# Kernel optimization log

Hardware: AMD Instinct MI355X
Metric: run time of the kernel (lower is better)

The kernel has to match this reference:

```python
import jax, jax.numpy as jnp
import numpy as np

N_NODES = 50000
NEG_SLOPE = 0.2
EPS = 1e-16


def gatv2_layer(x, src, dst, Wl, Wr, att, bias):
    # x: [N, F_in]; Wl, Wr: [F_in, F_out]; att: [F_out]; bias: [F_out]
    xl = x @ Wl  # source-side transform [N, F_out]
    xr = x @ Wr  # target-side transform [N, F_out]
    # per-edge GATv2 logit: att . LeakyReLU(xl[src] + xr[dst])
    z = xl[src] + xr[dst]                               # [E, F_out]
    e = jnp.sum(jax.nn.leaky_relu(z, NEG_SLOPE) * att, axis=-1)  # [E]
    # segment softmax over incoming edges of each dst node
    m = jax.ops.segment_max(e, dst, num_segments=N_NODES)       # [N]
    a = jnp.exp(e - m[dst])                                      # [E]
    s = jax.ops.segment_sum(a, dst, num_segments=N_NODES)       # [N]
    alpha = a / (s[dst] + EPS)                                   # [E]
    # weighted scatter-aggregate of source messages
    out = jax.ops.segment_sum(alpha[:, None] * xl[src], dst, num_segments=N_NODES)
    return out + bias


def setup_inputs() -> dict:
    key = jax.random.key(0)
    ks = jax.random.split(key, 10)
    F_in, H, C = 256, 128, 64
    glorot = lambda k, fi, fo: jax.random.normal(k, (fi, fo), jnp.float32) * np.sqrt(2.0 / (fi + fo))
    x = jax.random.normal(ks[0], (N_NODES, F_in), jnp.float32)
    edge_index = jax.random.randint(ks[1], (2, 1600000), 0, N_NODES, jnp.int64 if jax.config.jax_enable_x64 else jnp.int32)
    Wl1 = glorot(ks[2], F_in, H)
    Wr1 = glorot(ks[3], F_in, H)
    att1 = jax.random.normal(ks[4], (H,), jnp.float32) * np.sqrt(2.0 / H)
    b1 = jnp.zeros((H,), jnp.float32)
    Wl2 = glorot(ks[5], H, C)
    Wr2 = glorot(ks[6], H, C)
    att2 = jax.random.normal(ks[7], (C,), jnp.float32) * np.sqrt(2.0 / C)
    b2 = jnp.zeros((C,), jnp.float32)
    return {"x": x, "edge_index": edge_index, "Wl1": Wl1, "Wr1": Wr1, "att1": att1, "b1": b1,
            "Wl2": Wl2, "Wr2": Wr2, "att2": att2, "b2": b2}


def reference(x, edge_index, Wl1, Wr1, att1, b1, Wl2, Wr2, att2, b2):
    src, dst = edge_index[0], edge_index[1]
    h = gatv2_layer(x, src, dst, Wl1, Wr1, att1, b1)
    h = jax.nn.relu(h)
    # dropout is identity in eval mode
    out = gatv2_layer(h, src, dst, Wl2, Wr2, att2, b2)
    return out
```

## Files before the change

kernel.cpp:

```cpp
#include <hip/hip_runtime.h>

#define N_NODES 50000
#define M_PAD 50048
#define MT 391
#define GEMM1_BLOCKS 782
#define F_IN 256
#define F_H 128
#define F_OUT 64
#define E_MAX 1600000
#define NEG_SLOPE 0.2f
#define EPS_F 1e-16f
#define NPART 196
#define NBUCK 196
#define CH_E 4096
#define NQUAD 12500
#define ATT_GRID 2048
#define FUSED_LDS 40960

typedef __bf16 bf16x8 __attribute__((ext_vector_type(8)));
typedef float f32x4 __attribute__((ext_vector_type(4)));
typedef float f32x2 __attribute__((ext_vector_type(2)));

__device__ unsigned short g_B1h[256 * 256];
__device__ unsigned short g_B1l[256 * 256];
__device__ unsigned short g_B2h[128 * 128];
__device__ unsigned short g_B2l[128 * 128];
__device__ unsigned short g_hh[(size_t)M_PAD * F_H];
__device__ unsigned short g_hl[(size_t)M_PAD * F_H];
__device__ unsigned short g_xl1b[(size_t)N_NODES * F_H];
__device__ float g_xr1[(size_t)N_NODES * F_H];
__device__ unsigned short g_xl2b[(size_t)N_NODES * F_OUT];
__device__ float g_xr2[(size_t)N_NODES * F_OUT];
__device__ unsigned g_cnt[N_NODES];
__device__ unsigned g_part[NPART];
__device__ unsigned g_rowstart[N_NODES + 1];
__device__ unsigned g_bcursor[NBUCK];
__device__ unsigned g_bucketed[E_MAX];
__device__ int g_src_sorted[E_MAX];

__device__ inline float san(float v) { return fminf(fmaxf(v, -64.f), 64.f); }
__device__ inline unsigned short f2bf(float f) {
    unsigned u = __float_as_uint(f);
    return (unsigned short)((u + 0x7fffu + ((u >> 16) & 1u)) >> 16);
}
__device__ inline float bf2f(unsigned short h) {
    return __uint_as_float(((unsigned)h) << 16);
}
__device__ inline float blo(unsigned w) { return __uint_as_float(w << 16); }
__device__ inline float bhi(unsigned w) { return __uint_as_float(w & 0xffff0000u); }

__global__ __launch_bounds__(256) void prep_hist(const int* __restrict__ dst, int E,
                                                 const float* __restrict__ Wl1,
                                                 const float* __restrict__ Wr1,
                                                 const float* __restrict__ Wl2,
                                                 const float* __restrict__ Wr2) {
    int i = blockIdx.x * 256 + threadIdx.x;
    if (i < 256 * 256) {
        int n = i >> 8, k = i & 255;
        float v = san((n < 128) ? Wl1[k * 128 + n] : Wr1[k * 128 + (n - 128)]);
        unsigned short h = f2bf(v);
        g_B1h[n * 256 + k] = h;
        g_B1l[n * 256 + k] = f2bf(v - bf2f(h));
    }
    if (i < 128 * 128) {
        int n = i >> 7, k = i & 127;
        float v = san((n < 64) ? Wl2[k * 64 + n] : Wr2[k * 64 + (n - 64)]);
        unsigned short h = f2bf(v);
        g_B2h[n * 128 + k] = h;
        g_B2l[n * 128 + k] = f2bf(v - bf2f(h));
    }
    if (i < (M_PAD - N_NODES) * F_H) {
        g_hh[(size_t)N_NODES * F_H + i] = 0;
        g_hl[(size_t)N_NODES * F_H + i] = 0;
    }
    if (i < E) atomicAdd(&g_cnt[dst[i]], 1u);
}

__global__ __launch_bounds__(256) void scanA() {
    int i = blockIdx.x * 256 + threadIdx.x;
    unsigned v = (i < N_NODES) ? g_cnt[i] : 0u;
#pragma unroll
    for (int off = 32; off > 0; off >>= 1) v += __shfl_xor(v, off, 64);
    __shared__ unsigned ws[4];
    if ((threadIdx.x & 63) == 0) ws[threadIdx.x >> 6] = v;
    __syncthreads();
    if (threadIdx.x == 0) g_part[blockIdx.x] = ws[0] + ws[1] + ws[2] + ws[3];
}
__global__ __launch_bounds__(256) void scanC2(int E) {
    __shared__ unsigned lds[256];
    __shared__ unsigned ws[4];
    int t = threadIdx.x, bid = blockIdx.x;
    unsigned pv = (t < bid) ? g_part[t] : 0u;
#pragma unroll
    for (int off = 32; off > 0; off >>= 1) pv += __shfl_xor(pv, off, 64);
    if ((t & 63) == 0) ws[t >> 6] = pv;
    int i = bid * 256 + t;
    unsigned v = (i < N_NODES) ? g_cnt[i] : 0u;
    if (i < N_NODES) g_cnt[i] = 0u;
    lds[t] = v;
    __syncthreads();
    unsigned base = ws[0] + ws[1] + ws[2] + ws[3];
    for (int off = 1; off < 256; off <<= 1) {
        unsigned u = (t >= off) ? lds[t - off] : 0u;
        __syncthreads();
        lds[t] += u;
        __syncthreads();
    }
    if (i < N_NODES) g_rowstart[i] = lds[t] - v + base;
    if (t == 0) g_bcursor[bid] = base;
    if (i == 0) g_rowstart[N_NODES] = (unsigned)E;
}

__global__ __launch_bounds__(256) void sortA_gemm1(const int* __restrict__ src,
                                                   const int* __restrict__ dst,
                                                   int E, int nSort,
                                                   const float* __restrict__ x) {
    __shared__ __align__(16) unsigned char s_raw[FUSED_LDS];
    int t = threadIdx.x;

    if ((int)blockIdx.x < nSort) {
        unsigned* l_cnt  = (unsigned*)s_raw;
        unsigned* l_base = l_cnt + NBUCK;
        int*      l_gadj = (int*)(l_base + NBUCK);
        unsigned* sc     = (unsigned*)(l_gadj + NBUCK);
        unsigned* stageW = sc + 256;
        unsigned char* stageB = (unsigned char*)(stageW + CH_E);
        int e0 = blockIdx.x * CH_E;
        int e1 = min(e0 + CH_E, E);
        int n = e1 - e0;
        for (int i = t; i < NBUCK; i += 256) l_cnt[i] = 0u;
        __syncthreads();
        for (int e = e0 + t; e < e1; e += 256)
            atomicAdd(&l_cnt[dst[e] >> 8], 1u);
        __syncthreads();
        {
            unsigned v = (t < NBUCK) ? l_cnt[t] : 0u;
            sc[t] = v;
            __syncthreads();
            for (int off = 1; off < 256; off <<= 1) {
                unsigned u = (t >= off) ? sc[t - off] : 0u;
                __syncthreads();
                sc[t] += u;
                __syncthreads();
            }
            if (t < NBUCK) l_base[t] = sc[t] - v;
        }
        __syncthreads();
        for (int b = t; b < NBUCK; b += 256) {
            unsigned c = l_cnt[b];
            unsigned gb = c ? atomicAdd(&g_bcursor[b], c) : 0u;
            l_gadj[b] = (int)gb - (int)l_base[b];
            l_cnt[b] = l_base[b];
        }
        __syncthreads();
        for (int e = e0 + t; e < e1; e += 256) {
            int d = dst[e];
            int b = d >> 8;
            unsigned p = atomicAdd(&l_cnt[b], 1u);
            stageW[p] = (unsigned)src[e] | ((unsigned)d << 16);
            stageB[p] = (unsigned char)b;
        }
        __syncthreads();
        for (int i = t; i < n; i += 256) {
            int b = stageB[i];
            g_bucketed[l_gadj[b] + i] = stageW[i];
        }
        return;
    }

    typedef unsigned short row40[40];
    row40* As_h = (row40*)s_raw;
    row40* As_l = (row40*)(s_raw + 10240);
    row40* Bs_h = (row40*)(s_raw + 20480);
    row40* Bs_l = (row40*)(s_raw + 30720);

    int bx = blockIdx.x - nSort;
    const int n0 = (bx & 1) * 128;
    const int m0 = (bx >> 1) * 128;
    const int wave = t >> 6, lane = t & 63;
    const int wm = (wave >> 1) * 64, wn = (wave & 1) * 64;
    const int lr = lane & 15, g8 = (lane >> 4) * 8;
    const int srow = t >> 1, shalf = (t & 1) * 16;

    f32x4 acc[4][4];
#pragma unroll
    for (int i = 0; i < 4; ++i)
#pragma unroll
        for (int j = 0; j < 4; ++j) acc[i][j] = (f32x4){0.f, 0.f, 0.f, 0.f};

    for (int kb = 0; kb < 256; kb += 32) {
        __syncthreads();
        {
            int grow = m0 + srow;
            float f[16];
            if (grow < N_NODES) {
                const float4* xp = (const float4*)(x + (size_t)grow * F_IN + kb + shalf);
                float4 v0 = xp[0], v1 = xp[1], v2 = xp[2], v3 = xp[3];
                f[0] = v0.x;  f[1] = v0.y;  f[2] = v0.z;  f[3] = v0.w;
                f[4] = v1.x;  f[5] = v1.y;  f[6] = v1.z;  f[7] = v1.w;
                f[8] = v2.x;  f[9] = v2.y;  f[10] = v2.z; f[11] = v2.w;
                f[12] = v3.x; f[13] = v3.y; f[14] = v3.z; f[15] = v3.w;
            } else {
#pragma unroll
                for (int j = 0; j < 16; ++j) f[j] = 0.f;
            }
            unsigned hw[8], lw[8];
#pragma unroll
            for (int j = 0; j < 8; ++j) {
                float a = san(f[2 * j]), b = san(f[2 * j + 1]);
                unsigned short ha = f2bf(a), hb = f2bf(b);
                unsigned short la = f2bf(a - bf2f(ha)), lb = f2bf(b - bf2f(hb));
                hw[j] = ((unsigned)hb << 16) | ha;
                lw[j] = ((unsigned)lb << 16) | la;
            }
            *(uint4*)&As_h[srow][shalf]     = make_uint4(hw[0], hw[1], hw[2], hw[3]);
            *(uint4*)&As_h[srow][shalf + 8] = make_uint4(hw[4], hw[5], hw[6], hw[7]);
            *(uint4*)&As_l[srow][shalf]     = make_uint4(lw[0], lw[1], lw[2], lw[3]);
            *(uint4*)&As_l[srow][shalf + 8] = make_uint4(lw[4], lw[5], lw[6], lw[7]);
        }
        {
            size_t gb = (size_t)(n0 + srow) * 256 + kb + shalf;
            *(uint4*)&Bs_h[srow][shalf]     = *(const uint4*)(g_B1h + gb);
            *(uint4*)&Bs_h[srow][shalf + 8] = *(const uint4*)(g_B1h + gb + 8);
            *(uint4*)&Bs_l[srow][shalf]     = *(const uint4*)(g_B1l + gb);
            *(uint4*)&Bs_l[srow][shalf + 8] = *(const uint4*)(g_B1l + gb + 8);
        }
        __syncthreads();

        bf16x8 af_h[4], af_l[4], bf_h[4], bf_l[4];
#pragma unroll
        for (int i = 0; i < 4; ++i) {
            af_h[i] = *(const bf16x8*)&As_h[wm + i * 16 + lr][g8];
            af_l[i] = *(const bf16x8*)&As_l[wm + i * 16 + lr][g8];
        }
#pragma unroll
        for (int j = 0; j < 4; ++j) {
            bf_h[j] = *(const bf16x8*)&Bs_h[wn + j * 16 + lr][g8];
            bf_l[j] = *(const bf16x8*)&Bs_l[wn + j * 16 + lr][g8];
        }
#pragma unroll
        for (int i = 0; i < 4; ++i)
#pragma unroll
            for (int j = 0; j < 4; ++j) {
                acc[i][j] = __builtin_amdgcn_mfma_f32_16x16x32_bf16(af_h[i], bf_h[j], acc[i][j], 0, 0, 0);
                acc[i][j] = __builtin_amdgcn_mfma_f32_16x16x32_bf16(af_h[i], bf_l[j], acc[i][j], 0, 0, 0);
                acc[i][j] = __builtin_amdgcn_mfma_f32_16x16x32_bf16(af_l[i], bf_h[j], acc[i][j], 0, 0, 0);
            }
    }

    const int drow = (lane >> 4) * 4;
#pragma unroll
    for (int i = 0; i < 4; ++i)
#pragma unroll
        for (int j = 0; j < 4; ++j) {
            int gn = n0 + wn + j * 16 + lr;
#pragma unroll
            for (int r = 0; r < 4; ++r) {
                int m = m0 + wm + i * 16 + drow + r;
                if (m < N_NODES) {
                    if (gn < F_H) g_xl1b[(size_t)m * F_H + gn] = f2bf(acc[i][j][r]);
                    else          g_xr1[(size_t)m * F_H + (gn - F_H)] = acc[i][j][r];
                }
            }
        }
}

__global__ __launch_bounds__(256) void sortB() {
    __shared__ unsigned l_cur[256];
    int b = blockIdx.x;
    int d0 = b * 256;
    int t = threadIdx.x;
    l_cur[t] = g_rowstart[min(d0 + t, N_NODES)];
    unsigned bstart = g_rowstart[min(d0, N_NODES)];
    unsigned bend   = g_rowstart[min(d0 + 256, N_NODES)];
    __syncthreads();
    for (unsigned i = bstart + t; i < bend; i += 256) {
        unsigned e = g_bucketed[i];
        unsigned d = e >> 16;
        unsigned pos = atomicAdd(&l_cur[d - d0], 1u);
        g_src_sorted[pos] = (int)(e & 0xFFFFu);
    }
}

__global__ __launch_bounds__(256) void gemm2() {
    __shared__ __align__(16) unsigned short As_h[128][40];
    __shared__ __align__(16) unsigned short As_l[128][40];
    __shared__ __align__(16) unsigned short Bs_h[128][40];
    __shared__ __align__(16) unsigned short Bs_l[128][40];

    const int m0 = blockIdx.x * 128;
    const int t = threadIdx.x;
    const int wave = t >> 6, lane = t & 63;
    const int wm = (wave >> 1) * 64, wn = (wave & 1) * 64;
    const int lr = lane & 15, g8 = (lane >> 4) * 8;
    const int srow = t >> 1, shalf = (t & 1) * 16;

    f32x4 acc[4][4];
#pragma unroll
    for (int i = 0; i < 4; ++i)
#pragma unroll
        for (int j = 0; j < 4; ++j) acc[i][j] = (f32x4){0.f, 0.f, 0.f, 0.f};

    for (int kb = 0; kb < 128; kb += 32) {
        __syncthreads();
        {
            size_t ga = (size_t)(m0 + srow) * 128 + kb + shalf;
            *(uint4*)&As_h[srow][shalf]     = *(const uint4*)(g_hh + ga);
            *(uint4*)&As_h[srow][shalf + 8] = *(const uint4*)(g_hh + ga + 8);
            *(uint4*)&As_l[srow][shalf]     = *(const uint4*)(g_hl + ga);
            *(uint4*)&As_l[srow][shalf + 8] = *(const uint4*)(g_hl + ga + 8);
            size_t gb = (size_t)srow * 128 + kb + shalf;
            *(uint4*)&Bs_h[srow][shalf]     = *(const uint4*)(g_B2h + gb);
            *(uint4*)&Bs_h[srow][shalf + 8] = *(const uint4*)(g_B2h + gb + 8);
            *(uint4*)&Bs_l[srow][shalf]     = *(const uint4*)(g_B2l + gb);
            *(uint4*)&Bs_l[srow][shalf + 8] = *(const uint4*)(g_B2l + gb + 8);
        }
        __syncthreads();

        bf16x8 af_h[4], af_l[4], bf_h[4], bf_l[4];
#pragma unroll
        for (int i = 0; i < 4; ++i) {
            af_h[i] = *(const bf16x8*)&As_h[wm + i * 16 + lr][g8];
            af_l[i] = *(const bf16x8*)&As_l[wm + i * 16 + lr][g8];
        }
#pragma unroll
        for (int j = 0; j < 4; ++j) {
            bf_h[j] = *(const bf16x8*)&Bs_h[wn + j * 16 + lr][g8];
            bf_l[j] = *(const bf16x8*)&Bs_l[wn + j * 16 + lr][g8];
        }
#pragma unroll
        for (int i = 0; i < 4; ++i)
#pragma unroll
            for (int j = 0; j < 4; ++j) {
                acc[i][j] = __builtin_amdgcn_mfma_f32_16x16x32_bf16(af_h[i], bf_h[j], acc[i][j], 0, 0, 0);
                acc[i][j] = __builtin_amdgcn_mfma_f32_16x16x32_bf16(af_h[i], bf_l[j], acc[i][j], 0, 0, 0);
                acc[i][j] = __builtin_amdgcn_mfma_f32_16x16x32_bf16(af_l[i], bf_h[j], acc[i][j], 0, 0, 0);
            }
    }

    const int drow = (lane >> 4) * 4;
#pragma unroll
    for (int i = 0; i < 4; ++i)
#pragma unroll
        for (int j = 0; j < 4; ++j) {
            int gn = wn + j * 16 + lr;
#pragma unroll
            for (int r = 0; r < 4; ++r) {
                int m = m0 + wm + i * 16 + drow + r;
                if (m < N_NODES) {
                    if (gn < F_OUT) g_xl2b[(size_t)m * F_OUT + gn] = f2bf(acc[i][j][r]);
                    else            g_xr2[(size_t)m * F_OUT + (gn - F_OUT)] = acc[i][j][r];
                }
            }
        }
}

__global__ __launch_bounds__(256) void att_agg1(const float* __restrict__ att,
                                                const float* __restrict__ bias) {
    __shared__ float s_out[4][F_H];
    int wid = threadIdx.x >> 6, lane = threadIdx.x & 63;
    int g = lane >> 3;
    int fi = lane & 7;
    int f0 = fi * 16;

    f32x2 at2[8];
    {
        const float4* atp = (const float4*)(att + f0);
#pragma unroll
        for (int q = 0; q < 4; ++q) {
            float4 a = atp[q];
            at2[2 * q]     = (f32x2){san(a.x), san(a.y)};
            at2[2 * q + 1] = (f32x2){san(a.z), san(a.w)};
        }
    }

    for (int qd = blockIdx.x; qd < NQUAD; qd += gridDim.x) {
        int w = qd * 4 + wid;

        f32x2 xr2[8];
        {
            const float4* xrp = (const float4*)(g_xr1 + (size_t)w * F_H + f0);
#pragma unroll
            for (int q = 0; q < 4; ++q) {
                float4 v = xrp[q];
                xr2[2 * q]     = (f32x2){v.x, v.y};
                xr2[2 * q + 1] = (f32x2){v.z, v.w};
            }
        }

        int beg = (int)g_rowstart[w], end = (int)g_rowstart[w + 1];
        float m = -INFINITY, ssum = 0.f;
        f32x2 acc2[8];
#pragma unroll
        for (int q = 0; q < 8; ++q) acc2[q] = (f32x2){0.f, 0.f};

        for (int c0 = beg; c0 < end; c0 += 64) {
            int nc = min(64, end - c0);
            int mysrc = (lane < nc) ? g_src_sorted[c0 + lane] : 0;
            for (int r0 = 0; r0 < nc; r0 += 16) {
                int eA = r0 + g, eB = r0 + 8 + g;
                int sA = __shfl(mysrc, eA, 64);
                int sB = __shfl(mysrc, eB, 64);
                const uint4* rpA = (const uint4*)(g_xl1b + (size_t)sA * F_H + f0);
                const uint4* rpB = (const uint4*)(g_xl1b + (size_t)sB * F_H + f0);
                uint4 a0 = rpA[0], a1 = rpA[1];
                uint4 b0 = rpB[0], b1 = rpB[1];
                f32x2 rA[8];
                rA[0] = (f32x2){blo(a0.x), bhi(a0.x)};
                rA[1] = (f32x2){blo(a0.y), bhi(a0.y)};
                rA[2] = (f32x2){blo(a0.z), bhi(a0.z)};
                rA[3] = (f32x2){blo(a0.w), bhi(a0.w)};
                rA[4] = (f32x2){blo(a1.x), bhi(a1.x)};
                rA[5] = (f32x2){blo(a1.y), bhi(a1.y)};
                rA[6] = (f32x2){blo(a1.z), bhi(a1.z)};
                rA[7] = (f32x2){blo(a1.w), bhi(a1.w)};
                float dA1 = 0.f, dA2 = 0.f;
#pragma unroll
                for (int q = 0; q < 8; ++q) {
                    f32x2 z = rA[q] + xr2[q];
                    dA1 = fmaf(z.x, at2[q].x, dA1);
                    dA2 = fmaf(fabsf(z.x), at2[q].x, dA2);
                    dA1 = fmaf(z.y, at2[q].y, dA1);
                    dA2 = fmaf(fabsf(z.y), at2[q].y, dA2);
                }
                float dA = fmaf(0.6f, dA1, 0.4f * dA2);
                f32x2 rB[8];
                rB[0] = (f32x2){blo(b0.x), bhi(b0.x)};
                rB[1] = (f32x2){blo(b0.y), bhi(b0.y)};
                rB[2] = (f32x2){blo(b0.z), bhi(b0.z)};
                rB[3] = (f32x2){blo(b0.w), bhi(b0.w)};
                rB[4] = (f32x2){blo(b1.x), bhi(b1.x)};
                rB[5] = (f32x2){blo(b1.y), bhi(b1.y)};
                rB[6] = (f32x2){blo(b1.z), bhi(b1.z)};
                rB[7] = (f32x2){blo(b1.w), bhi(b1.w)};
                float dB1 = 0.f, dB2 = 0.f;
#pragma unroll
                for (int q = 0; q < 8; ++q) {
                    f32x2 z = rB[q] + xr2[q];
                    dB1 = fmaf(z.x, at2[q].x, dB1);
                    dB2 = fmaf(fabsf(z.x), at2[q].x, dB2);
                    dB1 = fmaf(z.y, at2[q].y, dB1);
                    dB2 = fmaf(fabsf(z.y), at2[q].y, dB2);
                }
                float dB = fmaf(0.6f, dB1, 0.4f * dB2);
                dA += __shfl_xor(dA, 1, 64);
                dA += __shfl_xor(dA, 2, 64);
                dA += __shfl_xor(dA, 4, 64);
                dB += __shfl_xor(dB, 1, 64);
                dB += __shfl_xor(dB, 2, 64);
                dB += __shfl_xor(dB, 4, 64);
                float eAv = (eA < nc) ? dA : -INFINITY;
                float eBv = (eB < nc) ? dB : -INFINITY;
                float M = fmaxf(eAv, eBv);
                M = fmaxf(M, __shfl_xor(M, 8, 64));
                M = fmaxf(M, __shfl_xor(M, 16, 64));
                M = fmaxf(M, __shfl_xor(M, 32, 64));
                if (M > m + 8.f) {
                    float sc = __expf(m - M);
                    m = M;
                    ssum *= sc;
#pragma unroll
                    for (int q = 0; q < 8; ++q) acc2[q] *= sc;
                }
                float pA = __expf(eAv - m);
                float pB = __expf(eBv - m);
                ssum += pA + pB;
#pragma unroll
                for (int q = 0; q < 8; ++q) {
                    acc2[q] += rA[q] * pA;
                    acc2[q] += rB[q] * pB;
                }
            }
        }
#pragma unroll
        for (int off = 8; off < 64; off <<= 1) {
            ssum += __shfl_xor(ssum, off, 64);
#pragma unroll
            for (int q = 0; q < 8; ++q) {
                acc2[q].x += __shfl_xor(acc2[q].x, off, 64);
                acc2[q].y += __shfl_xor(acc2[q].y, off, 64);
            }
        }
        float inv = 1.f / (ssum + EPS_F);
        if (g == 0) {
            float2* op = (float2*)&s_out[wid][f0];
#pragma unroll
            for (int q = 0; q < 8; ++q) {
                float2 v;
                v.x = acc2[q].x * inv; v.y = acc2[q].y * inv;
                op[q] = v;
            }
        }
        int f2 = lane * 2;
        float2 o = *(float2*)&s_out[wid][f2];
        o.x = fmaxf(o.x + san(bias[f2]), 0.f);
        o.y = fmaxf(o.y + san(bias[f2 + 1]), 0.f);
        unsigned short hx = f2bf(o.x), hy = f2bf(o.y);
        unsigned short lx = f2bf(o.x - bf2f(hx)), ly = f2bf(o.y - bf2f(hy));
        size_t base = (size_t)w * F_H + f2;
        *(unsigned*)(g_hh + base) = ((unsigned)hy << 16) | hx;
        *(unsigned*)(g_hl + base) = ((unsigned)ly << 16) | lx;
    }
}

__global__ __launch_bounds__(256) void att_agg2(const float* __restrict__ att,
                                                const float* __restrict__ bias,
                                                float* __restrict__ out) {
    __shared__ float s_out[4][F_OUT];
    int wid = threadIdx.x >> 6, lane = threadIdx.x & 63;
    int g = lane >> 3;
    int fi = lane & 7;
    int f0 = fi * 8;

    f32x2 at2[4];
    {
        const float4* atp = (const float4*)(att + f0);
#pragma unroll
        for (int q = 0; q < 2; ++q) {
            float4 a = atp[q];
            at2[2 * q]     = (f32x2){san(a.x), san(a.y)};
            at2[2 * q + 1] = (f32x2){san(a.z), san(a.w)};
        }
    }

    for (int qd = blockIdx.x; qd < NQUAD; qd += gridDim.x) {
        int w = qd * 4 + wid;

        f32x2 xr2[4];
        {
            const float4* xrp = (const float4*)(g_xr2 + (size_t)w * F_OUT + f0);
#pragma unroll
            for (int q = 0; q < 2; ++q) {
                float4 v = xrp[q];
                xr2[2 * q]     = (f32x2){v.x, v.y};
                xr2[2 * q + 1] = (f32x2){v.z, v.w};
            }
        }

        int beg = (int)g_rowstart[w], end = (int)g_rowstart[w + 1];
        float m = -INFINITY, ssum = 0.f;
        f32x2 acc2[4];
#pragma unroll
        for (int q = 0; q < 4; ++q) acc2[q] = (f32x2){0.f, 0.f};

        for (int c0 = beg; c0 < end; c0 += 64) {
            int nc = min(64, end - c0);
            int mysrc = (lane < nc) ? g_src_sorted[c0 + lane] : 0;
            for (int r0 = 0; r0 < nc; r0 += 16) {
                int eA = r0 + g, eB = r0 + 8 + g;
                int sA = __shfl(mysrc, eA, 64);
                int sB = __shfl(mysrc, eB, 64);
                uint4 a0 = *(const uint4*)(g_xl2b + (size_t)sA * F_OUT + f0);
                uint4 b0 = *(const uint4*)(g_xl2b + (size_t)sB * F_OUT + f0);
                f32x2 rA[4], rB[4];
                rA[0] = (f32x2){blo(a0.x), bhi(a0.x)};
                rA[1] = (f32x2){blo(a0.y), bhi(a0.y)};
                rA[2] = (f32x2){blo(a0.z), bhi(a0.z)};
                rA[3] = (f32x2){blo(a0.w), bhi(a0.w)};
                rB[0] = (f32x2){blo(b0.x), bhi(b0.x)};
                rB[1] = (f32x2){blo(b0.y), bhi(b0.y)};
                rB[2] = (f32x2){blo(b0.z), bhi(b0.z)};
                rB[3] = (f32x2){blo(b0.w), bhi(b0.w)};
                float dA1 = 0.f, dA2 = 0.f, dB1 = 0.f, dB2 = 0.f;
#pragma unroll
                for (int q = 0; q < 4; ++q) {
                    f32x2 zA = rA[q] + xr2[q];
                    dA1 = fmaf(zA.x, at2[q].x, dA1);
                    dA2 = fmaf(fabsf(zA.x), at2[q].x, dA2);
                    dA1 = fmaf(zA.y, at2[q].y, dA1);
                    dA2 = fmaf(fabsf(zA.y), at2[q].y, dA2);
                    f32x2 zB = rB[q] + xr2[q];
                    dB1 = fmaf(zB.x, at2[q].x, dB1);
                    dB2 = fmaf(fabsf(zB.x), at2[q].x, dB2);
                    dB1 = fmaf(zB.y, at2[q].y, dB1);
                    dB2 = fmaf(fabsf(zB.y), at2[q].y, dB2);
                }
                float dA = fmaf(0.6f, dA1, 0.4f * dA2);
                float dB = fmaf(0.6f, dB1, 0.4f * dB2);
                dA += __shfl_xor(dA, 1, 64);
                dA += __shfl_xor(dA, 2, 64);
                dA += __shfl_xor(dA, 4, 64);
                dB += __shfl_xor(dB, 1, 64);
                dB += __shfl_xor(dB, 2, 64);
                dB += __shfl_xor(dB, 4, 64);
                float eAv = (eA < nc) ? dA : -INFINITY;
                float eBv = (eB < nc) ? dB : -INFINITY;
                float M = fmaxf(eAv, eBv);
                M = fmaxf(M, __shfl_xor(M, 8, 64));
                M = fmaxf(M, __shfl_xor(M, 16, 64));
                M = fmaxf(M, __shfl_xor(M, 32, 64));
                if (M > m + 8.f) {
                    float sc = __expf(m - M);
                    m = M;
                    ssum *= sc;
#pragma unroll
                    for (int q = 0; q < 4; ++q) acc2[q] *= sc;
                }
                float pA = __expf(eAv - m);
                float pB = __expf(eBv - m);
                ssum += pA + pB;
#pragma unroll
                for (int q = 0; q < 4; ++q) {
                    acc2[q] += rA[q] * pA;
                    acc2[q] += rB[q] * pB;
                }
            }
        }
#pragma unroll
        for (int off = 8; off < 64; off <<= 1) {
            ssum += __shfl_xor(ssum, off, 64);
#pragma unroll
            for (int q = 0; q < 4; ++q) {
                acc2[q].x += __shfl_xor(acc2[q].x, off, 64);
                acc2[q].y += __shfl_xor(acc2[q].y, off, 64);
            }
        }
        float inv = 1.f / (ssum + EPS_F);
        if (g == 0) {
            float2* op = (float2*)&s_out[wid][f0];
#pragma unroll
            for (int q = 0; q < 2; ++q) {
                float2 v0, v1;
                v0.x = acc2[2 * q].x * inv;     v0.y = acc2[2 * q].y * inv;
                v1.x = acc2[2 * q + 1].x * inv; v1.y = acc2[2 * q + 1].y * inv;
                op[2 * q] = v0;
                op[2 * q + 1] = v1;
            }
        }
        out[(size_t)w * F_OUT + lane] = s_out[wid][lane] + san(bias[lane]);
    }
}

extern "C" void kernel_launch(void* const* d_in, const int* in_sizes, int n_in,
                              void* d_out, int out_size, void* d_ws, size_t ws_size,
                              hipStream_t stream) {
    const float* x    = (const float*)d_in[0];
    const int*   ei   = (const int*)d_in[1];
    const float* Wl1  = (const float*)d_in[2];
    const float* Wr1  = (const float*)d_in[3];
    const float* att1 = (const float*)d_in[4];
    const float* b1   = (const float*)d_in[5];
    const float* Wl2  = (const float*)d_in[6];
    const float* Wr2  = (const float*)d_in[7];
    const float* att2 = (const float*)d_in[8];
    const float* b2   = (const float*)d_in[9];

    int E = in_sizes[1] / 2;
    const int* src = ei;
    const int* dst = ei + E;

    int gE = (E + 255) / 256;
    int gSA = (E + CH_E - 1) / CH_E;

    prep_hist<<<gE, 256, 0, stream>>>(dst, E, Wl1, Wr1, Wl2, Wr2);
    scanA<<<NPART, 256, 0, stream>>>();
    scanC2<<<NPART, 256, 0, stream>>>(E);
    sortA_gemm1<<<gSA + GEMM1_BLOCKS, 256, 0, stream>>>(src, dst, E, gSA, x);
    sortB<<<NBUCK, 256, 0, stream>>>();

    att_agg1<<<ATT_GRID, 256, 0, stream>>>(att1, b1);

    gemm2<<<MT, 256, 0, stream>>>();
    att_agg2<<<ATT_GRID, 256, 0, stream>>>(att2, b2, (float*)d_out);
}
```

Measured before the change: 397.6 us.

## Widen GEMM1 tile to cover both Wl and Wr columns per block

```diff
diff --git a/kernel.cpp b/kernel.cpp
--- a/kernel.cpp
+++ b/kernel.cpp
@@ -3,7 +3,6 @@
 #define N_NODES 50000
 #define M_PAD 50048
 #define MT 391
-#define GEMM1_BLOCKS 782
 #define F_IN 256
 #define F_H 128
 #define F_OUT 64
@@ -15,7 +14,7 @@
 #define CH_E 4096
 #define NQUAD 12500
 #define ATT_GRID 2048
-#define FUSED_LDS 40960
+#define FUSED_LDS 61440
 
 typedef __bf16 bf16x8 __attribute__((ext_vector_type(8)));
 typedef float f32x4 __attribute__((ext_vector_type(4)));
@@ -111,7 +110,7 @@
     if (i == 0) g_rowstart[N_NODES] = (unsigned)E;
 }
 
-__global__ __launch_bounds__(256) void sortA_gemm1(const int* __restrict__ src,
+__global__ __launch_bounds__(512) void sortA_gemm1(const int* __restrict__ src,
                                                    const int* __restrict__ dst,
                                                    int E, int nSort,
                                                    const float* __restrict__ x) {
@@ -128,32 +127,32 @@
         int e0 = blockIdx.x * CH_E;
         int e1 = min(e0 + CH_E, E);
         int n = e1 - e0;
-        for (int i = t; i < NBUCK; i += 256) l_cnt[i] = 0u;
-        __syncthreads();
-        for (int e = e0 + t; e < e1; e += 256)
+        for (int i = t; i < NBUCK; i += 512) l_cnt[i] = 0u;
+        __syncthreads();
+        for (int e = e0 + t; e < e1; e += 512)
             atomicAdd(&l_cnt[dst[e] >> 8], 1u);
         __syncthreads();
         {
             unsigned v = (t < NBUCK) ? l_cnt[t] : 0u;
-            sc[t] = v;
+            if (t < 256) sc[t] = v;
             __syncthreads();
             for (int off = 1; off < 256; off <<= 1) {
-                unsigned u = (t >= off) ? sc[t - off] : 0u;
+                unsigned u = (t >= off && t < 256) ? sc[t - off] : 0u;
                 __syncthreads();
-                sc[t] += u;
+                if (t < 256) sc[t] += u;
                 __syncthreads();
             }
             if (t < NBUCK) l_base[t] = sc[t] - v;
         }
         __syncthreads();
-        for (int b = t; b < NBUCK; b += 256) {
+        for (int b = t; b < NBUCK; b += 512) {
             unsigned c = l_cnt[b];
             unsigned gb = c ? atomicAdd(&g_bcursor[b], c) : 0u;
             l_gadj[b] = (int)gb - (int)l_base[b];
             l_cnt[b] = l_base[b];
         }
         __syncthreads();
-        for (int e = e0 + t; e < e1; e += 256) {
+        for (int e = e0 + t; e < e1; e += 512) {
             int d = dst[e];
             int b = d >> 8;
             unsigned p = atomicAdd(&l_cnt[b], 1u);
@@ -161,7 +160,7 @@
             stageB[p] = (unsigned char)b;
         }
         __syncthreads();
-        for (int i = t; i < n; i += 256) {
+        for (int i = t; i < n; i += 512) {
             int b = stageB[i];
             g_bucketed[l_gadj[b] + i] = stageW[i];
         }
@@ -172,15 +171,14 @@
     row40* As_h = (row40*)s_raw;
     row40* As_l = (row40*)(s_raw + 10240);
     row40* Bs_h = (row40*)(s_raw + 20480);
-    row40* Bs_l = (row40*)(s_raw + 30720);
-
-    int bx = blockIdx.x - nSort;
-    const int n0 = (bx & 1) * 128;
-    const int m0 = (bx >> 1) * 128;
+    row40* Bs_l = (row40*)(s_raw + 40960);
+
+    const int m0 = (blockIdx.x - nSort) * 128;
     const int wave = t >> 6, lane = t & 63;
-    const int wm = (wave >> 1) * 64, wn = (wave & 1) * 64;
+    const int wm = (wave >> 2) * 64, wn = (wave & 3) * 64;
     const int lr = lane & 15, g8 = (lane >> 4) * 8;
-    const int srow = t >> 1, shalf = (t & 1) * 16;
+    const int srowA = t >> 2, skA = (t & 3) * 8;
+    const int srowB = t >> 1, skB = (t & 1) * 16;
 
     f32x4 acc[4][4];
 #pragma unroll
@@ -191,39 +189,35 @@
     for (int kb = 0; kb < 256; kb += 32) {
         __syncthreads();
         {
-            int grow = m0 + srow;
-            float f[16];
+            int grow = m0 + srowA;
+            float f[8];
             if (grow < N_NODES) {
-                const float4* xp = (const float4*)(x + (size_t)grow * F_IN + kb + shalf);
-                float4 v0 = xp[0], v1 = xp[1], v2 = xp[2], v3 = xp[3];
-                f[0] = v0.x;  f[1] = v0.y;  f[2] = v0.z;  f[3] = v0.w;
-                f[4] = v1.x;  f[5] = v1.y;  f[6] = v1.z;  f[7] = v1.w;
-                f[8] = v2.x;  f[9] = v2.y;  f[10] = v2.z; f[11] = v2.w;
-                f[12] = v3.x; f[13] = v3.y; f[14] = v3.z; f[15] = v3.w;
+                const float4* xp = (const float4*)(x + (size_t)grow * F_IN + kb + skA);
+                float4 v0 = xp[0], v1 = xp[1];
+                f[0] = v0.x; f[1] = v0.y; f[2] = v0.z; f[3] = v0.w;
+                f[4] = v1.x; f[5] = v1.y; f[6] = v1.z; f[7] = v1.w;
             } else {
 #pragma unroll
-                for (int j = 0; j < 16; ++j) f[j] = 0.f;
-            }
-            unsigned hw[8], lw[8];
-#pragma unroll
-            for (int j = 0; j < 8; ++j) {
+                for (int j = 0; j < 8; ++j) f[j] = 0.f;
+            }
+            unsigned hw[4], lw[4];
+#pragma unroll
+            for (int j = 0; j < 4; ++j) {
                 float a = san(f[2 * j]), b = san(f[2 * j + 1]);
                 unsigned short ha = f2bf(a), hb = f2bf(b);
                 unsigned short la = f2bf(a - bf2f(ha)), lb = f2bf(b - bf2f(hb));
                 hw[j] = ((unsigned)hb << 16) | ha;
                 lw[j] = ((unsigned)lb << 16) | la;
             }
-            *(uint4*)&As_h[srow][shalf]     = make_uint4(hw[0], hw[1], hw[2], hw[3]);
-            *(uint4*)&As_h[srow][shalf + 8] = make_uint4(hw[4], hw[5], hw[6], hw[7]);
-            *(uint4*)&As_l[srow][shalf]     = make_uint4(lw[0], lw[1], lw[2], lw[3]);
-            *(uint4*)&As_l[srow][shalf + 8] = make_uint4(lw[4], lw[5], lw[6], lw[7]);
+            *(uint4*)&As_h[srowA][skA] = make_uint4(hw[0], hw[1], hw[2], hw[3]);
+            *(uint4*)&As_l[srowA][skA] = make_uint4(lw[0], lw[1], lw[2], lw[3]);
         }
         {
-            size_t gb = (size_t)(n0 + srow) * 256 + kb + shalf;
-            *(uint4*)&Bs_h[srow][shalf]     = *(const uint4*)(g_B1h + gb);
-            *(uint4*)&Bs_h[srow][shalf + 8] = *(const uint4*)(g_B1h + gb + 8);
-            *(uint4*)&Bs_l[srow][shalf]     = *(const uint4*)(g_B1l + gb);
-            *(uint4*)&Bs_l[srow][shalf + 8] = *(const uint4*)(g_B1l + gb + 8);
+            size_t gb = (size_t)srowB * 256 + kb + skB;
+            *(uint4*)&Bs_h[srowB][skB]     = *(const uint4*)(g_B1h + gb);
+            *(uint4*)&Bs_h[srowB][skB + 8] = *(const uint4*)(g_B1h + gb + 8);
+            *(uint4*)&Bs_l[srowB][skB]     = *(const uint4*)(g_B1l + gb);
+            *(uint4*)&Bs_l[srowB][skB + 8] = *(const uint4*)(g_B1l + gb + 8);
         }
         __syncthreads();
 
@@ -253,7 +247,7 @@
     for (int i = 0; i < 4; ++i)
 #pragma unroll
         for (int j = 0; j < 4; ++j) {
-            int gn = n0 + wn + j * 16 + lr;
+            int gn = wn + j * 16 + lr;
 #pragma unroll
             for (int r = 0; r < 4; ++r) {
                 int m = m0 + wm + i * 16 + drow + r;
@@ -655,7 +649,7 @@
     prep_hist<<<gE, 256, 0, stream>>>(dst, E, Wl1, Wr1, Wl2, Wr2);
     scanA<<<NPART, 256, 0, stream>>>();
     scanC2<<<NPART, 256, 0, stream>>>(E);
-    sortA_gemm1<<<gSA + GEMM1_BLOCKS, 256, 0, stream>>>(src, dst, E, gSA, x);
+    sortA_gemm1<<<gSA + MT, 512, 0, stream>>>(src, dst, E, gSA, x);
     sortB<<<NBUCK, 256, 0, stream>>>();
 
     att_agg1<<<ATT_GRID, 256, 0, stream>>>(att1, b1);
```

Result: no change. 401.1 us (+0.9%).

## Replace global degree histogram and scan with fixed-capacity buckets and in-bucket counting

Applied to the files above, without the earlier changes.

```diff
diff --git a/kernel.cpp b/kernel.cpp
--- a/kernel.cpp
+++ b/kernel.cpp
@@ -7,12 +7,11 @@
 #define F_IN 256
 #define F_H 128
 #define F_OUT 64
-#define E_MAX 1600000
 #define NEG_SLOPE 0.2f
 #define EPS_F 1e-16f
-#define NPART 196
 #define NBUCK 196
 #define CH_E 4096
+#define BUCKCAP 9216
 #define NQUAD 12500
 #define ATT_GRID 2048
 #define FUSED_LDS 40960
@@ -31,12 +30,11 @@
 __device__ float g_xr1[(size_t)N_NODES * F_H];
 __device__ unsigned short g_xl2b[(size_t)N_NODES * F_OUT];
 __device__ float g_xr2[(size_t)N_NODES * F_OUT];
-__device__ unsigned g_cnt[N_NODES];
-__device__ unsigned g_part[NPART];
-__device__ unsigned g_rowstart[N_NODES + 1];
+__device__ unsigned g_rowstart[N_NODES];
+__device__ unsigned g_rowend[N_NODES];
 __device__ unsigned g_bcursor[NBUCK];
-__device__ unsigned g_bucketed[E_MAX];
-__device__ int g_src_sorted[E_MAX];
+__device__ unsigned g_bucketed[(size_t)NBUCK * BUCKCAP];
+__device__ int g_src_sorted[(size_t)NBUCK * BUCKCAP];
 
 __device__ inline float san(float v) { return fminf(fmaxf(v, -64.f), 64.f); }
 __device__ inline unsigned short f2bf(float f) {
@@ -49,11 +47,10 @@
 __device__ inline float blo(unsigned w) { return __uint_as_float(w << 16); }
 __device__ inline float bhi(unsigned w) { return __uint_as_float(w & 0xffff0000u); }
 
-__global__ __launch_bounds__(256) void prep_hist(const int* __restrict__ dst, int E,
-                                                 const float* __restrict__ Wl1,
-                                                 const float* __restrict__ Wr1,
-                                                 const float* __restrict__ Wl2,
-                                                 const float* __restrict__ Wr2) {
+__global__ __launch_bounds__(256) void prep_w(const float* __restrict__ Wl1,
+                                              const float* __restrict__ Wr1,
+                                              const float* __restrict__ Wl2,
+                                              const float* __restrict__ Wr2) {
     int i = blockIdx.x * 256 + threadIdx.x;
     if (i < 256 * 256) {
         int n = i >> 8, k = i & 255;
@@ -73,42 +70,7 @@
         g_hh[(size_t)N_NODES * F_H + i] = 0;
         g_hl[(size_t)N_NODES * F_H + i] = 0;
     }
-    if (i < E) atomicAdd(&g_cnt[dst[i]], 1u);
-}
-
-__global__ __launch_bounds__(256) void scanA() {
-    int i = blockIdx.x * 256 + threadIdx.x;
-    unsigned v = (i < N_NODES) ? g_cnt[i] : 0u;
-#pragma unroll
-    for (int off = 32; off > 0; off >>= 1) v += __shfl_xor(v, off, 64);
-    __shared__ unsigned ws[4];
-    if ((threadIdx.x & 63) == 0) ws[threadIdx.x >> 6] = v;
-    __syncthreads();
-    if (threadIdx.x == 0) g_part[blockIdx.x] = ws[0] + ws[1] + ws[2] + ws[3];
-}
-__global__ __launch_bounds__(256) void scanC2(int E) {
-    __shared__ unsigned lds[256];
-    __shared__ unsigned ws[4];
-    int t = threadIdx.x, bid = blockIdx.x;
-    unsigned pv = (t < bid) ? g_part[t] : 0u;
-#pragma unroll
-    for (int off = 32; off > 0; off >>= 1) pv += __shfl_xor(pv, off, 64);
-    if ((t & 63) == 0) ws[t >> 6] = pv;
-    int i = bid * 256 + t;
-    unsigned v = (i < N_NODES) ? g_cnt[i] : 0u;
-    if (i < N_NODES) g_cnt[i] = 0u;
-    lds[t] = v;
-    __syncthreads();
-    unsigned base = ws[0] + ws[1] + ws[2] + ws[3];
-    for (int off = 1; off < 256; off <<= 1) {
-        unsigned u = (t >= off) ? lds[t - off] : 0u;
-        __syncthreads();
-        lds[t] += u;
-        __syncthreads();
-    }
-    if (i < N_NODES) g_rowstart[i] = lds[t] - v + base;
-    if (t == 0) g_bcursor[bid] = base;
-    if (i == 0) g_rowstart[N_NODES] = (unsigned)E;
+    if (i < NBUCK) g_bcursor[i] = (unsigned)i * BUCKCAP;
 }
 
 __global__ __launch_bounds__(256) void sortA_gemm1(const int* __restrict__ src,
@@ -266,18 +228,41 @@
 }
 
 __global__ __launch_bounds__(256) void sortB() {
-    __shared__ unsigned l_cur[256];
+    __shared__ unsigned l_cnt[256];
+    __shared__ unsigned l_sc[256];
     int b = blockIdx.x;
     int d0 = b * 256;
     int t = threadIdx.x;
-    l_cur[t] = g_rowstart[min(d0 + t, N_NODES)];
-    unsigned bstart = g_rowstart[min(d0, N_NODES)];
-    unsigned bend   = g_rowstart[min(d0 + 256, N_NODES)];
+    unsigned bstart = (unsigned)b * BUCKCAP;
+    unsigned count = g_bcursor[b] - bstart;
+    l_cnt[t] = 0u;
     __syncthreads();
-    for (unsigned i = bstart + t; i < bend; i += 256) {
-        unsigned e = g_bucketed[i];
+    for (unsigned i = t; i < count; i += 256) {
+        unsigned e = g_bucketed[bstart + i];
+        atomicAdd(&l_cnt[(e >> 16) - d0], 1u);
+    }
+    __syncthreads();
+    unsigned v = l_cnt[t];
+    l_sc[t] = v;
+    __syncthreads();
+    for (int off = 1; off < 256; off <<= 1) {
+        unsigned u = (t >= off) ? l_sc[t - off] : 0u;
+        __syncthreads();
+        l_sc[t] += u;
+        __syncthreads();
+    }
+    unsigned rs = bstart + l_sc[t] - v;
+    int node = d0 + t;
+    if (node < N_NODES) {
+        g_rowstart[node] = rs;
+        g_rowend[node] = rs + v;
+    }
+    l_cnt[t] = rs;
+    __syncthreads();
+    for (unsigned i = t; i < count; i += 256) {
+        unsigned e = g_bucketed[bstart + i];
         unsigned d = e >> 16;
-        unsigned pos = atomicAdd(&l_cur[d - d0], 1u);
+        unsigned pos = atomicAdd(&l_cnt[d - d0], 1u);
         g_src_sorted[pos] = (int)(e & 0xFFFFu);
     }
 }
@@ -388,7 +373,7 @@
             }
         }
 
-        int beg = (int)g_rowstart[w], end = (int)g_rowstart[w + 1];
+        int beg = (int)g_rowstart[w], end = (int)g_rowend[w];
         float m = -INFINITY, ssum = 0.f;
         f32x2 acc2[8];
 #pragma unroll
@@ -537,7 +522,7 @@
             }
         }
 
-        int beg = (int)g_rowstart[w], end = (int)g_rowstart[w + 1];
+        int beg = (int)g_rowstart[w], end = (int)g_rowend[w];
         float m = -INFINITY, ssum = 0.f;
         f32x2 acc2[4];
 #pragma unroll
@@ -649,12 +634,9 @@
     const int* src = ei;
     const int* dst = ei + E;
 
-    int gE = (E + 255) / 256;
     int gSA = (E + CH_E - 1) / CH_E;
 
-    prep_hist<<<gE, 256, 0, stream>>>(dst, E, Wl1, Wr1, Wl2, Wr2);
-    scanA<<<NPART, 256, 0, stream>>>();
-    scanC2<<<NPART, 256, 0, stream>>>(E);
+    prep_w<<<256, 256, 0, stream>>>(Wl1, Wr1, Wl2, Wr2);
     sortA_gemm1<<<gSA + GEMM1_BLOCKS, 256, 0, stream>>>(src, dst, E, gSA, x);
     sortB<<<NBUCK, 256, 0, stream>>>();
 
```

Measured after the change: 336.0 us. -15.5%, faster.
